# Performance work log

Measured on AMD Instinct MI355X. Metric: run time of the kernel, lower is better.

The kernel has to match this reference:

```python
import jax, jax.numpy as jnp
from jax import lax
import numpy as np

K = 3          # kernel size
PAD = 1
DIL = 1
INIT_OFFSET = 0.5
CLAMP_MIN, CLAMP_MAX = 0.0, 1.0


def _kernel_grid():
    # ordering along X fastest: (0,0),(1,0),(2,0),(0,1),... last dim = (x, y)
    k = jnp.arange(K * K)
    kx = (k % K).astype(jnp.float32)
    ky = (k // K).astype(jnp.float32)
    return jnp.stack([kx, ky], axis=-1)  # (9, 2)


def _bilinear(img, py, px):
    """img: (C,H,W); py,px: (n,H,W) sampling locations -> (C,n,H,W), zeros outside."""
    H, W = img.shape[1], img.shape[2]
    y0 = jnp.floor(py); x0 = jnp.floor(px)
    y1 = y0 + 1.0;      x1 = x0 + 1.0
    wy1 = py - y0; wy0 = 1.0 - wy1
    wx1 = px - x0; wx0 = 1.0 - wx1

    def g(yi, xi):
        yc = jnp.clip(yi, 0, H - 1).astype(jnp.int32)
        xc = jnp.clip(xi, 0, W - 1).astype(jnp.int32)
        valid = ((yi >= 0) & (yi <= H - 1) & (xi >= 0) & (xi <= W - 1)).astype(img.dtype)
        return img[:, yc, xc] * valid[None]  # (C,n,H,W)

    return (g(y0, x0) * (wy0 * wx0)[None] + g(y0, x1) * (wy0 * wx1)[None]
            + g(y1, x0) * (wy1 * wx0)[None] + g(y1, x1) * (wy1 * wx1)[None])


def setup_inputs() -> dict:
    key = jax.random.key(0)
    k1, k2, k3 = jax.random.split(key, 3)
    B, C, O, H, W = 4, 64, 64, 128, 128
    x = jax.random.normal(k1, (B, C, H, W), jnp.float32)
    w_off = 0.05 * jax.random.normal(k2, (1, C, K, K), jnp.float32)   # lie-weight predictor
    w_conv = 0.05 * jax.random.normal(k3, (O, C, K, K), jnp.float32)  # deform conv weight
    # dominant homography dom = P diag(d) Pinv with positive eigenvalues (eig done offline,
    # matching torch.linalg.eig of the constant gd_homo buffer)
    rng = np.random.default_rng(0)
    P = rng.normal(size=(3, 3)).astype(np.float32) + 3.0 * np.eye(3, dtype=np.float32)
    Pinv = np.linalg.inv(P).astype(np.float32)
    d = np.array([1.15, 1.05, 1.0], np.float32)
    return {"x": x, "w_off": w_off, "w_conv": w_conv,
            "P": jnp.asarray(P), "d": jnp.asarray(d), "Pinv": jnp.asarray(Pinv)}


def reference(x, w_off, w_conv, P, d, Pinv):
    B, C, H, W = x.shape
    O = w_conv.shape[0]
    n = K * K
    # 1) per-pixel Lie coefficients
    raw = lax.conv_general_dilated(x, w_off, (1, 1), ((PAD, PAD), (PAD, PAD)),
                                   dimension_numbers=("NCHW", "OIHW", "NCHW"))[:, 0]  # (B,H,W)
    lw = jnp.clip(raw + INIT_OFFSET, CLAMP_MIN, CLAMP_MAX).reshape(-1)  # (M,)
    # 2) lie_weights_to_hom: Hom = P diag(d**lw) Pinv per pixel
    pw = d[None, :] ** lw[:, None]                       # (M,3)
    Hom = jnp.einsum("ik,mk,kj->mij", P, pw, Pinv)      # (M,3,3)
    # 3) hom_to_grid_offset (pix_grid=None path)
    kg = _kernel_grid()                                  # (9,2) (x,y)
    center = (K - 1) / 2.0
    pts = jnp.concatenate([kg - center, jnp.ones((n, 1), jnp.float32)], axis=-1)  # (9,3)
    q = jnp.einsum("mij,nj->mni", Hom, pts)             # (M,9,3)
    out_grid = q[..., :2] / q[..., 2:3] + center         # (M,9,2)
    goff = (out_grid - kg[None]).reshape(B, H, W, n, 2)  # (B,H,W,9,2) (dx,dy)
    # 4) grid_offset_to_deform_offset: swap to (dy,dx), layout (B,n,H,W)
    dy = goff[..., 1].transpose(0, 3, 1, 2)
    dx = goff[..., 0].transpose(0, 3, 1, 2)
    k = jnp.arange(n)
    ky = (k // K).astype(x.dtype); kx = (k % K).astype(x.dtype)
    iy = jnp.arange(H, dtype=x.dtype); ix = jnp.arange(W, dtype=x.dtype)
    py = dy + (iy[None, None, :, None] - PAD + DIL * ky[None, :, None, None])
    px = dx + (ix[None, None, None, :] - PAD + DIL * kx[None, :, None, None])
    # 5) deformable conv: bilinear gather then contraction with weights
    sampled = jax.vmap(_bilinear)(x, py, px)             # (B,C,9,H,W)
    out = jnp.einsum("bcnhw,ocn->bohw", sampled, w_conv.reshape(O, C, n))
    return out
```

## Files before the change

kernel.cpp:

```cpp
#include <hip/hip_runtime.h>
#include <hip/hip_bf16.h>

#define BN 4
#define CN 64
#define ON 64
#define HN 128
#define WN 128
#define HWN (HN*WN)
#define NT 9

typedef __attribute__((ext_vector_type(8))) short bf16x8;
typedef __attribute__((ext_vector_type(4))) float floatx4;

static __device__ __forceinline__ unsigned short f2bf(float f) {
    unsigned int u = __builtin_bit_cast(unsigned int, f);
    u += 0x7fffu + ((u >> 16) & 1u);
    return (unsigned short)(u >> 16);
}
static __device__ __forceinline__ float bf2f(short h) {
    unsigned int u = ((unsigned int)(unsigned short)h) << 16;
    return __builtin_bit_cast(float, u);
}

static __device__ __forceinline__ int swz_work(int b) {
    return ((b & 7) << 7) | (b >> 3);
}

__global__ __launch_bounds__(256) void transpose_kernel(
    const float* __restrict__ x, unsigned short* __restrict__ xTh)
{
    __shared__ float ls[64][65];
    const int tid   = threadIdx.x;
    const int work  = swz_work(blockIdx.x);
    const int pbase = work << 6;
    const int bi    = pbase >> 14;
    const int poff  = pbase & (HWN-1);
    const float* xb = x + (size_t)bi*CN*HWN + poff;
    const int lane = tid & 63, g = tid >> 6;

    #pragma unroll
    for (int k = 0; k < 16; ++k) {
        int c = g*16 + k;
        ls[c][lane] = xb[(size_t)c*HWN + lane];
    }
    __syncthreads();

    unsigned short* dst = xTh + (size_t)pbase*CN;
    #pragma unroll
    for (int j = 0; j < 2; ++j) {
        int u   = j*256 + tid;
        int p   = u >> 3;
        int c8i = (u & 7)*8;
        unsigned int a = (unsigned int)f2bf(ls[c8i+0][p]) | ((unsigned int)f2bf(ls[c8i+1][p])<<16);
        unsigned int b = (unsigned int)f2bf(ls[c8i+2][p]) | ((unsigned int)f2bf(ls[c8i+3][p])<<16);
        unsigned int c = (unsigned int)f2bf(ls[c8i+4][p]) | ((unsigned int)f2bf(ls[c8i+5][p])<<16);
        unsigned int e = (unsigned int)f2bf(ls[c8i+6][p]) | ((unsigned int)f2bf(ls[c8i+7][p])<<16);
        ((uint4*)dst)[u] = make_uint4(a,b,c,e);
    }
}

__global__ __launch_bounds__(256) void offsets_kernel(
    const float* __restrict__ x, const float* __restrict__ w_off,
    const float* __restrict__ w_conv,
    const float* __restrict__ P, const float* __restrict__ d,
    const float* __restrict__ Pinv,
    float2* __restrict__ offs, unsigned short* __restrict__ wbf)
{
    const int tid = threadIdx.x;
    __shared__ float swoff[CN*NT];
    __shared__ float sred[4][64];
    __shared__ float sHm[64][10];

    for (int i = tid; i < CN*NT; i += 256) swoff[i] = w_off[i];

    int gid = blockIdx.x * 256 + tid;
    if (gid < ON*CN*NT) {
        int o   = gid / (CN*NT);
        int rem = gid - o*(CN*NT);
        int c   = rem / NT;
        int n   = rem - c*NT;
        wbf[(n*ON + o)*CN + c] = f2bf(w_conv[gid]);
    }

    const int work  = swz_work(blockIdx.x);
    const int pbase = work << 6;
    const int pix   = tid & 63;
    const int cg    = tid >> 6;
    const int p     = pbase + pix;
    const int wi    = p & (WN-1);
    const int hi    = (p >> 7) & (HN-1);
    const int bi    = p >> 14;
    const float* xb   = x + (size_t)bi*CN*HWN + (size_t)(cg*16)*HWN;
    const float* swc0 = &swoff[cg*16*NT];

    __syncthreads();

    float accv = 0.f;
    #pragma unroll
    for (int ky = 0; ky < 3; ++ky) {
        int yy = hi + ky - 1;
        #pragma unroll
        for (int kx = 0; kx < 3; ++kx) {
            int xx = wi + kx - 1;
            bool v  = (yy >= 0) && (yy < HN) && (xx >= 0) && (xx < WN);
            float m = v ? 1.f : 0.f;
            int a   = v ? (yy*WN + xx) : 0;
            const float* swc = swc0 + (ky*3 + kx);
            float t0 = 0.f, t1 = 0.f, t2 = 0.f, t3 = 0.f;
            #pragma unroll
            for (int c = 0; c < 16; c += 4) {
                t0 = fmaf(xb[(size_t)(c+0)*HWN + a], swc[(c+0)*NT], t0);
                t1 = fmaf(xb[(size_t)(c+1)*HWN + a], swc[(c+1)*NT], t1);
                t2 = fmaf(xb[(size_t)(c+2)*HWN + a], swc[(c+2)*NT], t2);
                t3 = fmaf(xb[(size_t)(c+3)*HWN + a], swc[(c+3)*NT], t3);
            }
            accv = fmaf(m, (t0+t1)+(t2+t3), accv);
        }
    }
    sred[cg][pix] = accv;
    __syncthreads();

    if (tid < 64) {
        float raw = (sred[0][tid]+sred[1][tid]) + (sred[2][tid]+sred[3][tid]);
        float lw  = fminf(fmaxf(raw + 0.5f, 0.f), 1.f);
        float pw[3];
        #pragma unroll
        for (int k = 0; k < 3; ++k) pw[k] = exp2f(lw * log2f(d[k]));
        #pragma unroll
        for (int i = 0; i < 3; ++i)
            #pragma unroll
            for (int j = 0; j < 3; ++j)
                sHm[tid][i*3+j] = P[i*3+0]*pw[0]*Pinv[0+j]
                                + P[i*3+1]*pw[1]*Pinv[3+j]
                                + P[i*3+2]*pw[2]*Pinv[6+j];
    }
    __syncthreads();

    for (int e = tid; e < 64*NT; e += 256) {
        int pp = e / NT, n = e - pp*NT;
        float fx = (float)(n % 3) - 1.f;
        float fy = (float)(n / 3) - 1.f;
        float qx = sHm[pp][0]*fx + sHm[pp][1]*fy + sHm[pp][2];
        float qy = sHm[pp][3]*fx + sHm[pp][4]*fy + sHm[pp][5];
        float qz = sHm[pp][6]*fx + sHm[pp][7]*fy + sHm[pp][8];
        float ri = 1.f / qz;
        offs[(size_t)(pbase+pp)*NT + n] = make_float2(qx*ri, qy*ri);
    }
}

#define LDSD 20736

__global__ __launch_bounds__(256) void deform_bf16(
    const unsigned short* __restrict__ xTh, const float2* __restrict__ offs,
    const unsigned short* __restrict__ wbf, float* __restrict__ out)
{
    __shared__ __align__(16) char lds[LDSD];
    int*            tapB = (int*)lds;
    float4*         tapW = (float4*)(lds + 2304);
    unsigned short* sT   = (unsigned short*)(lds + 11520);

    const int tid   = threadIdx.x;
    const int work  = swz_work(blockIdx.x);
    const int pbase = work << 6;
    const int w0    = pbase & (WN-1);
    const int hi    = (pbase >> 7) & (HN-1);
    const int bi    = pbase >> 14;
    const unsigned short* xb = xTh + (size_t)bi * HWN * CN;

    for (int e = tid; e < 64*NT; e += 256) {
        int pix = e / NT, n = e - pix*NT;
        float2 off = offs[(size_t)(pbase + pix)*NT + n];
        float px = (float)(w0 + pix) + off.x;
        float py = (float)hi + off.y;
        float x0f = floorf(px), y0f = floorf(py);
        float fx = px - x0f,    fy = py - y0f;
        int ix0 = (int)x0f, iy0 = (int)y0f;
        int bx = min(max(ix0, 0), WN-2);
        int by = min(max(iy0, 0), HN-2);
        float wx0 = 1.f - fx, wx1 = fx;
        float wy0 = 1.f - fy, wy1 = fy;
        float sxL = (ix0   == bx   ? wx0 : 0.f) + (ix0+1 == bx   ? wx1 : 0.f);
        float sxR = (ix0   == bx+1 ? wx0 : 0.f) + (ix0+1 == bx+1 ? wx1 : 0.f);
        float syT = (iy0   == by   ? wy0 : 0.f) + (iy0+1 == by   ? wy1 : 0.f);
        float syB = (iy0   == by+1 ? wy0 : 0.f) + (iy0+1 == by+1 ? wy1 : 0.f);
        tapB[e] = (by*WN + bx)*CN;
        tapW[e] = make_float4(syT*sxL, syT*sxR, syB*sxL, syB*sxR);
    }
    __syncthreads();

    const int lane = tid & 63;
    const int g    = tid >> 6;
    const int p8   = lane & 7;
    const int c8   = lane >> 3;
    const int q    = lane >> 4;
    const int m15  = lane & 15;
    const int mpix = g*16 + m15;

    floatx4 acc[4];
    #pragma unroll
    for (int f = 0; f < 4; ++f) acc[f] = (floatx4){0.f,0.f,0.f,0.f};

    for (int n = 0; n < NT; ++n) {
        #pragma unroll
        for (int i = 0; i < 2; ++i) {
            int bp = g*16 + i*8 + p8;
            int e  = bp*NT + n;
            int tb = tapB[e];
            float4 tw = tapW[e];
            const unsigned short* A = xb + (size_t)tb + c8*8;
            bf16x8 v00 = *(const bf16x8*)A;
            bf16x8 v01 = *(const bf16x8*)(A + CN);
            bf16x8 v10 = *(const bf16x8*)(A + WN*CN);
            bf16x8 v11 = *(const bf16x8*)(A + WN*CN + CN);
            unsigned int pk[4];
            #pragma unroll
            for (int j = 0; j < 8; j += 2) {
                float a0 = fmaf(tw.x, bf2f(v00[j]),
                           fmaf(tw.y, bf2f(v01[j]),
                           fmaf(tw.z, bf2f(v10[j]), tw.w*bf2f(v11[j]))));
                float a1 = fmaf(tw.x, bf2f(v00[j+1]),
                           fmaf(tw.y, bf2f(v01[j+1]),
                           fmaf(tw.z, bf2f(v10[j+1]), tw.w*bf2f(v11[j+1]))));
                pk[j>>1] = (unsigned int)f2bf(a0) | ((unsigned int)f2bf(a1)<<16);
            }
            *(int4*)&sT[bp*72 + c8*8] = make_int4(pk[0],pk[1],pk[2],pk[3]);
        }
        #pragma unroll
        for (int k0 = 0; k0 < 64; k0 += 32) {
            bf16x8 a = *(const bf16x8*)&sT[mpix*72 + k0 + q*8];
            #pragma unroll
            for (int f = 0; f < 4; ++f) {
                bf16x8 bfr = *(const bf16x8*)&wbf[((size_t)(n*ON + f*16 + m15))*CN + k0 + q*8];
                acc[f] = __builtin_amdgcn_mfma_f32_16x16x32_bf16(a, bfr, acc[f], 0, 0, 0);
            }
        }
    }

    __syncthreads();
    float* tr = (float*)lds;
    #pragma unroll
    for (int f = 0; f < 4; ++f) {
        int o = f*16 + m15;
        #pragma unroll
        for (int r = 0; r < 4; ++r) {
            int pix = g*16 + q*4 + r;
            tr[o*72 + pix] = acc[f][r];
        }
    }
    __syncthreads();
    const int og = tid >> 6;
    float* ob = out + (((size_t)bi*ON)*HN + hi)*WN + w0;
    #pragma unroll
    for (int j = 0; j < 16; ++j) {
        int o = og*16 + j;
        ob[(size_t)o*HWN + lane] = tr[o*72 + lane];
    }
}

extern "C" void kernel_launch(void* const* d_in, const int* in_sizes, int n_in,
                              void* d_out, int out_size, void* d_ws, size_t ws_size,
                              hipStream_t stream) {
    const float* x      = (const float*)d_in[0];
    const float* w_off  = (const float*)d_in[1];
    const float* w_conv = (const float*)d_in[2];
    const float* P      = (const float*)d_in[3];
    const float* d      = (const float*)d_in[4];
    const float* Pinv   = (const float*)d_in[5];
    float* out = (float*)d_out;

    const size_t XTH_BYTES  = (size_t)BN*HN*WN*CN*2;
    const size_t OFFS_BYTES = (size_t)BN*HWN*NT*8;

    unsigned short* xTh = (unsigned short*)d_ws;
    float2* offs = (float2*)((char*)d_ws + XTH_BYTES);
    unsigned short* wbf = (unsigned short*)((char*)d_ws + XTH_BYTES + OFFS_BYTES);

    transpose_kernel<<<1024, 256, 0, stream>>>(x, xTh);
    offsets_kernel<<<1024, 256, 0, stream>>>(x, w_off, w_conv, P, d, Pinv, offs, wbf);
    deform_bf16<<<1024, 256, 0, stream>>>(xTh, offs, wbf, out);
}
```

Before: 157.4 us.

## Fuse transpose into offsets kernel via LDS row tiles and gather fp32 taps

The separate transpose kernel is merged into the offsets kernel. Each block stages three padded input rows in LDS, uses them both for the 3x3 offset-predictor convolution and to write a channel-last copy of x. That copy is now fp32 instead of bf16. The deform kernel gathers float4 corners per lane and converts to bf16 only after interpolation. This removes one launch and the repeated global reads in the offset conv, but doubles the bytes of the intermediate tensor and of the gather traffic in the main kernel.

```diff
diff --git a/kernel.cpp b/kernel.cpp
--- a/kernel.cpp
+++ b/kernel.cpp
@@ -17,60 +17,25 @@
     u += 0x7fffu + ((u >> 16) & 1u);
     return (unsigned short)(u >> 16);
 }
-static __device__ __forceinline__ float bf2f(short h) {
-    unsigned int u = ((unsigned int)(unsigned short)h) << 16;
-    return __builtin_bit_cast(float, u);
-}
 
 static __device__ __forceinline__ int swz_work(int b) {
     return ((b & 7) << 7) | (b >> 3);
 }
 
-__global__ __launch_bounds__(256) void transpose_kernel(
-    const float* __restrict__ x, unsigned short* __restrict__ xTh)
-{
-    __shared__ float ls[64][65];
-    const int tid   = threadIdx.x;
-    const int work  = swz_work(blockIdx.x);
-    const int pbase = work << 6;
-    const int bi    = pbase >> 14;
-    const int poff  = pbase & (HWN-1);
-    const float* xb = x + (size_t)bi*CN*HWN + poff;
-    const int lane = tid & 63, g = tid >> 6;
-
-    #pragma unroll
-    for (int k = 0; k < 16; ++k) {
-        int c = g*16 + k;
-        ls[c][lane] = xb[(size_t)c*HWN + lane];
-    }
-    __syncthreads();
-
-    unsigned short* dst = xTh + (size_t)pbase*CN;
-    #pragma unroll
-    for (int j = 0; j < 2; ++j) {
-        int u   = j*256 + tid;
-        int p   = u >> 3;
-        int c8i = (u & 7)*8;
-        unsigned int a = (unsigned int)f2bf(ls[c8i+0][p]) | ((unsigned int)f2bf(ls[c8i+1][p])<<16);
-        unsigned int b = (unsigned int)f2bf(ls[c8i+2][p]) | ((unsigned int)f2bf(ls[c8i+3][p])<<16);
-        unsigned int c = (unsigned int)f2bf(ls[c8i+4][p]) | ((unsigned int)f2bf(ls[c8i+5][p])<<16);
-        unsigned int e = (unsigned int)f2bf(ls[c8i+6][p]) | ((unsigned int)f2bf(ls[c8i+7][p])<<16);
-        ((uint4*)dst)[u] = make_uint4(a,b,c,e);
-    }
-}
-
-__global__ __launch_bounds__(256) void offsets_kernel(
+__global__ __launch_bounds__(256) void to_kernel(
     const float* __restrict__ x, const float* __restrict__ w_off,
     const float* __restrict__ w_conv,
     const float* __restrict__ P, const float* __restrict__ d,
     const float* __restrict__ Pinv,
-    float2* __restrict__ offs, unsigned short* __restrict__ wbf)
+    float* __restrict__ xT, float2* __restrict__ offs,
+    unsigned short* __restrict__ wbf)
 {
-    const int tid = threadIdx.x;
+    __shared__ float ls[3][64][68];
     __shared__ float swoff[CN*NT];
     __shared__ float sred[4][64];
     __shared__ float sHm[64][10];
 
+    const int tid = threadIdx.x;
     for (int i = tid; i < CN*NT; i += 256) swoff[i] = w_off[i];
 
     int gid = blockIdx.x * 256 + tid;
@@ -84,40 +49,65 @@
 
     const int work  = swz_work(blockIdx.x);
     const int pbase = work << 6;
-    const int pix   = tid & 63;
-    const int cg    = tid >> 6;
-    const int p     = pbase + pix;
-    const int wi    = p & (WN-1);
-    const int hi    = (p >> 7) & (HN-1);
-    const int bi    = p >> 14;
-    const float* xb   = x + (size_t)bi*CN*HWN + (size_t)(cg*16)*HWN;
-    const float* swc0 = &swoff[cg*16*NT];
-
-    __syncthreads();
-
-    float accv = 0.f;
-    #pragma unroll
-    for (int ky = 0; ky < 3; ++ky) {
-        int yy = hi + ky - 1;
-        #pragma unroll
-        for (int kx = 0; kx < 3; ++kx) {
-            int xx = wi + kx - 1;
-            bool v  = (yy >= 0) && (yy < HN) && (xx >= 0) && (xx < WN);
-            float m = v ? 1.f : 0.f;
-            int a   = v ? (yy*WN + xx) : 0;
-            const float* swc = swc0 + (ky*3 + kx);
-            float t0 = 0.f, t1 = 0.f, t2 = 0.f, t3 = 0.f;
+    const int w0    = pbase & (WN-1);
+    const int hi    = (pbase >> 7) & (HN-1);
+    const int bi    = pbase >> 14;
+    const float* xb = x + (size_t)bi * CN * HWN;
+
+    #pragma unroll
+    for (int r = 0; r < 3; ++r) {
+        int yy = min(max(hi - 1 + r, 0), HN - 1);
+        const float* rowp = xb + (size_t)yy * WN;
+        for (int j = tid; j < 64*66; j += 256) {
+            int c   = j / 66;
+            int col = j - c*66;
+            int xg  = min(max(w0 - 1 + col, 0), WN - 1);
+            ls[r][c][col] = rowp[(size_t)c*HWN + xg];
+        }
+    }
+    __syncthreads();
+
+    {
+        float4* dst = (float4*)(xT + (size_t)pbase*CN);
+        #pragma unroll
+        for (int j = 0; j < 4; ++j) {
+            int f4 = j*256 + tid;
+            int p  = f4 >> 4;
+            int c4 = (f4 & 15)*4;
+            dst[f4] = make_float4(ls[1][c4+0][p+1], ls[1][c4+1][p+1],
+                                  ls[1][c4+2][p+1], ls[1][c4+3][p+1]);
+        }
+    }
+
+    {
+        const int pix = tid & 63;
+        const int cg  = tid >> 6;
+        const int wi  = w0 + pix;
+        const float* swc0 = &swoff[cg*16*NT];
+        float accv = 0.f;
+        #pragma unroll
+        for (int ky = 0; ky < 3; ++ky) {
+            int yy = hi + ky - 1;
             #pragma unroll
-            for (int c = 0; c < 16; c += 4) {
-                t0 = fmaf(xb[(size_t)(c+0)*HWN + a], swc[(c+0)*NT], t0);
-                t1 = fmaf(xb[(size_t)(c+1)*HWN + a], swc[(c+1)*NT], t1);
-                t2 = fmaf(xb[(size_t)(c+2)*HWN + a], swc[(c+2)*NT], t2);
-                t3 = fmaf(xb[(size_t)(c+3)*HWN + a], swc[(c+3)*NT], t3);
+            for (int kx = 0; kx < 3; ++kx) {
+                int xx = wi + kx - 1;
+                bool v  = (yy >= 0) && (yy < HN) && (xx >= 0) && (xx < WN);
+                float m = v ? 1.f : 0.f;
+                int lcol = pix + kx;
+                const float* swc = swc0 + (ky*3 + kx);
+                float t0 = 0.f, t1 = 0.f, t2 = 0.f, t3 = 0.f;
+                #pragma unroll
+                for (int c = 0; c < 16; c += 4) {
+                    t0 = fmaf(ls[ky][cg*16 + c+0][lcol], swc[(c+0)*NT], t0);
+                    t1 = fmaf(ls[ky][cg*16 + c+1][lcol], swc[(c+1)*NT], t1);
+                    t2 = fmaf(ls[ky][cg*16 + c+2][lcol], swc[(c+2)*NT], t2);
+                    t3 = fmaf(ls[ky][cg*16 + c+3][lcol], swc[(c+3)*NT], t3);
+                }
+                accv = fmaf(m, (t0+t1)+(t2+t3), accv);
             }
-            accv = fmaf(m, (t0+t1)+(t2+t3), accv);
-        }
-    }
-    sred[cg][pix] = accv;
+        }
+        sred[cg][pix] = accv;
+    }
     __syncthreads();
 
     if (tid < 64) {
@@ -148,13 +138,13 @@
     }
 }
 
-#define LDSD 20736
-
-__global__ __launch_bounds__(256) void deform_bf16(
-    const unsigned short* __restrict__ xTh, const float2* __restrict__ offs,
+#define LDSB 20736
+
+__global__ __launch_bounds__(256) void deform_xt(
+    const float* __restrict__ xT, const float2* __restrict__ offs,
     const unsigned short* __restrict__ wbf, float* __restrict__ out)
 {
-    __shared__ __align__(16) char lds[LDSD];
+    __shared__ __align__(16) char lds[LDSB];
     int*            tapB = (int*)lds;
     float4*         tapW = (float4*)(lds + 2304);
     unsigned short* sT   = (unsigned short*)(lds + 11520);
@@ -165,7 +155,7 @@
     const int w0    = pbase & (WN-1);
     const int hi    = (pbase >> 7) & (HN-1);
     const int bi    = pbase >> 14;
-    const unsigned short* xb = xTh + (size_t)bi * HWN * CN;
+    const float* xTb = xT + (size_t)bi * HWN * CN;
 
     for (int e = tid; e < 64*NT; e += 256) {
         int pix = e / NT, n = e - pix*NT;
@@ -190,40 +180,35 @@
 
     const int lane = tid & 63;
     const int g    = tid >> 6;
-    const int p8   = lane & 7;
-    const int c8   = lane >> 3;
     const int q    = lane >> 4;
     const int m15  = lane & 15;
     const int mpix = g*16 + m15;
+    const int psub = lane >> 4;
+    const int k4   = (lane & 15)*4;
 
     floatx4 acc[4];
     #pragma unroll
     for (int f = 0; f < 4; ++f) acc[f] = (floatx4){0.f,0.f,0.f,0.f};
 
     for (int n = 0; n < NT; ++n) {
-        #pragma unroll
-        for (int i = 0; i < 2; ++i) {
-            int bp = g*16 + i*8 + p8;
-            int e  = bp*NT + n;
+        #pragma unroll 2
+        for (int s = 0; s < 4; ++s) {
+            int p = g*16 + s*4 + psub;
+            int e = p*NT + n;
             int tb = tapB[e];
             float4 tw = tapW[e];
-            const unsigned short* A = xb + (size_t)tb + c8*8;
-            bf16x8 v00 = *(const bf16x8*)A;
-            bf16x8 v01 = *(const bf16x8*)(A + CN);
-            bf16x8 v10 = *(const bf16x8*)(A + WN*CN);
-            bf16x8 v11 = *(const bf16x8*)(A + WN*CN + CN);
-            unsigned int pk[4];
-            #pragma unroll
-            for (int j = 0; j < 8; j += 2) {
-                float a0 = fmaf(tw.x, bf2f(v00[j]),
-                           fmaf(tw.y, bf2f(v01[j]),
-                           fmaf(tw.z, bf2f(v10[j]), tw.w*bf2f(v11[j]))));
-                float a1 = fmaf(tw.x, bf2f(v00[j+1]),
-                           fmaf(tw.y, bf2f(v01[j+1]),
-                           fmaf(tw.z, bf2f(v10[j+1]), tw.w*bf2f(v11[j+1]))));
-                pk[j>>1] = (unsigned int)f2bf(a0) | ((unsigned int)f2bf(a1)<<16);
-            }
-            *(int4*)&sT[bp*72 + c8*8] = make_int4(pk[0],pk[1],pk[2],pk[3]);
+            const float* A = xTb + tb + k4;
+            float4 v00 = *(const float4*)A;
+            float4 v01 = *(const float4*)(A + CN);
+            float4 v10 = *(const float4*)(A + WN*CN);
+            float4 v11 = *(const float4*)(A + WN*CN + CN);
+            float rx = fmaf(tw.x,v00.x, fmaf(tw.y,v01.x, fmaf(tw.z,v10.x, tw.w*v11.x)));
+            float ry = fmaf(tw.x,v00.y, fmaf(tw.y,v01.y, fmaf(tw.z,v10.y, tw.w*v11.y)));
+            float rz = fmaf(tw.x,v00.z, fmaf(tw.y,v01.z, fmaf(tw.z,v10.z, tw.w*v11.z)));
+            float rw = fmaf(tw.x,v00.w, fmaf(tw.y,v01.w, fmaf(tw.z,v10.w, tw.w*v11.w)));
+            unsigned int u0 = (unsigned int)f2bf(rx) | ((unsigned int)f2bf(ry) << 16);
+            unsigned int u1 = (unsigned int)f2bf(rz) | ((unsigned int)f2bf(rw) << 16);
+            *(uint2*)&sT[p*72 + k4] = make_uint2(u0, u1);
         }
         #pragma unroll
         for (int k0 = 0; k0 < 64; k0 += 32) {
@@ -268,14 +253,13 @@
     const float* Pinv   = (const float*)d_in[5];
     float* out = (float*)d_out;
 
-    const size_t XTH_BYTES  = (size_t)BN*HN*WN*CN*2;
+    const size_t XT_BYTES   = (size_t)BN*HN*WN*CN*4;
     const size_t OFFS_BYTES = (size_t)BN*HWN*NT*8;
 
-    unsigned short* xTh = (unsigned short*)d_ws;
-    float2* offs = (float2*)((char*)d_ws + XTH_BYTES);
-    unsigned short* wbf = (unsigned short*)((char*)d_ws + XTH_BYTES + OFFS_BYTES);
-
-    transpose_kernel<<<1024, 256, 0, stream>>>(x, xTh);
-    offsets_kernel<<<1024, 256, 0, stream>>>(x, w_off, w_conv, P, d, Pinv, offs, wbf);
-    deform_bf16<<<1024, 256, 0, stream>>>(xTh, offs, wbf, out);
-}
+    float*  xT  = (float*)d_ws;
+    float2* offs = (float2*)((char*)d_ws + XT_BYTES);
+    unsigned short* wbf = (unsigned short*)((char*)d_ws + XT_BYTES + OFFS_BYTES);
+
+    to_kernel<<<1024, 256, 0, stream>>>(x, w_off, w_conv, P, d, Pinv, xT, offs, wbf);
+    deform_xt<<<1024, 256, 0, stream>>>(xT, offs, wbf, out);
+}
```

After: 151.0 us. -4.1%, faster.
